# Performance work log

Measured on AMD Instinct MI355X. Metric: run time of the kernel, lower is better.

The kernel has to match this reference:

```python
import jax, jax.numpy as jnp
import numpy as np

N_NODES = 50000
N_EDGES = 800000
IN_F = 128
HID_F = 128
OUT_F = 128

def safediv(a, b):
    b = jnp.where(b == 0, jnp.ones_like(b), b)
    return a / b

def setup_inputs() -> dict:
    key = jax.random.key(0)
    ks = jax.random.split(key, 8)
    h = jax.random.normal(ks[0], (N_NODES, IN_F), dtype=jnp.float32)
    ppr_weight = jax.random.uniform(ks[1], (N_EDGES,), dtype=jnp.float32)
    Qw = jax.random.normal(ks[2], (HID_F, IN_F), dtype=jnp.float32) * (1.0 / np.sqrt(IN_F))
    Qb = jnp.zeros((HID_F,), dtype=jnp.float32)
    Ww = jax.random.normal(ks[3], (OUT_F, IN_F + HID_F), dtype=jnp.float32) * (1.0 / np.sqrt(IN_F + HID_F))
    Wb = jnp.zeros((OUT_F,), dtype=jnp.float32)
    src = jax.random.randint(ks[4], (N_EDGES,), 0, N_NODES, dtype=jnp.int64 if jax.config.jax_enable_x64 else jnp.int32)
    dst = jax.random.randint(ks[5], (N_EDGES,), 0, N_NODES, dtype=jnp.int64 if jax.config.jax_enable_x64 else jnp.int32)
    return {"h": h, "ppr_weight": ppr_weight, "Qw": Qw, "Qb": Qb, "Ww": Ww, "Wb": Wb, "src": src, "dst": dst}

def reference(h, ppr_weight, Qw, Qb, Ww, Wb, src, dst):
    # neighbor transform: Q(h) -> [N, HID_F]
    hq = h @ Qw.T + Qb
    # message: h_w = hq[src] * ppr_weight  (edge-weighted gather) [E, HID_F]
    msg = hq[src] * ppr_weight[:, None]
    # reduce: scatter-sum messages and weights onto dst nodes
    h_agg = jax.ops.segment_sum(msg, dst, num_segments=N_NODES)
    w = jax.ops.segment_sum(ppr_weight, dst, num_segments=N_NODES)
    # apply: PPR-weighted mean, concat, linear, leaky_relu, L2 normalize
    h_agg = safediv(h_agg, w[:, None])
    h_concat = jnp.concatenate([h, h_agg], axis=1)
    h_new = jax.nn.leaky_relu(h_concat @ Ww.T + Wb, negative_slope=0.01)
    norm = jnp.linalg.norm(h_new, axis=1, keepdims=True)
    return safediv(h_new, norm)
```

## Files before the change

kernel.cpp:

```cpp
#include <hip/hip_runtime.h>
#include <stdint.h>

#define N_NODES 50000
#define N_EDGES 800000
#define IN_F 128
#define HID_F 128
#define OUT_F 128
#define CAT_F 256

#define NB 256
#define CHUNK 3136
#define NBUCK 3125
#define BCAP 384

typedef __bf16 bf16x8 __attribute__((ext_vector_type(8)));
typedef float f32x4 __attribute__((ext_vector_type(4)));

__device__ __forceinline__ uint32_t f2b(float f) {
  uint32_t u = __float_as_uint(f);
  return (u + 0x7fffu + ((u >> 16) & 1u)) >> 16;
}

__global__ void __launch_bounds__(256) prep_hist_kernel(
    const int* __restrict__ dst, int* __restrict__ G, const float* __restrict__ h,
    const float* __restrict__ Qw, const float* __restrict__ Ww, uint16_t* __restrict__ hB,
    uint16_t* __restrict__ QwB, uint16_t* __restrict__ WwB) {
  if (blockIdx.x < NB) {
    __shared__ int hist[NBUCK];
    for (int k = threadIdx.x; k < NBUCK; k += 256) hist[k] = 0;
    __syncthreads();
    int b = blockIdx.x;
    int base = b * CHUNK;
    int end = (base + CHUNK < N_EDGES) ? (base + CHUNK) : N_EDGES;
    for (int i4 = base / 4 + threadIdx.x; i4 * 4 < end; i4 += 256) {
      int4 d4 = ((const int4*)dst)[i4];
      atomicAdd(&hist[d4.x >> 4], 1);
      atomicAdd(&hist[d4.y >> 4], 1);
      atomicAdd(&hist[d4.z >> 4], 1);
      atomicAdd(&hist[d4.w >> 4], 1);
    }
    __syncthreads();
    for (int k = threadIdx.x; k < NBUCK; k += 256) G[(size_t)b * NBUCK + k] = hist[k];
  } else {
    const int TOT4 = (N_NODES * IN_F + HID_F * IN_F + OUT_F * CAT_F) / 4;
    int i4 = (blockIdx.x - NB) * 256 + threadIdx.x;
    if (i4 >= TOT4) return;
    int base = i4 * 4;
    const float* srcp;
    uint16_t* dstp;
    int off;
    if (base < N_NODES * IN_F) {
      srcp = h; dstp = hB; off = base;
    } else if (base < N_NODES * IN_F + HID_F * IN_F) {
      srcp = Qw; dstp = QwB; off = base - N_NODES * IN_F;
    } else {
      srcp = Ww; dstp = WwB; off = base - N_NODES * IN_F - HID_F * IN_F;
    }
    float4 v = *(const float4*)(srcp + off);
    ushort4 o;
    o.x = (uint16_t)f2b(v.x); o.y = (uint16_t)f2b(v.y);
    o.z = (uint16_t)f2b(v.z); o.w = (uint16_t)f2b(v.w);
    *(ushort4*)(dstp + off) = o;
  }
}

__global__ void __launch_bounds__(256) colscan_kernel(int* __restrict__ G,
                                                      int* __restrict__ cnt) {
  int w = (blockIdx.x * 256 + (int)threadIdx.x) >> 6;
  if (w >= NBUCK) return;
  int lane = threadIdx.x & 63;
  int v0 = G[(size_t)(4 * lane + 0) * NBUCK + w];
  int v1 = G[(size_t)(4 * lane + 1) * NBUCK + w];
  int v2 = G[(size_t)(4 * lane + 2) * NBUCK + w];
  int v3 = G[(size_t)(4 * lane + 3) * NBUCK + w];
  int s = v0 + v1 + v2 + v3;
  int inc = s;
#pragma unroll
  for (int d = 1; d < 64; d <<= 1) {
    int x = __shfl_up(inc, d, 64);
    if (lane >= d) inc += x;
  }
  int exc = inc - s;
  G[(size_t)(4 * lane + 0) * NBUCK + w] = exc;
  G[(size_t)(4 * lane + 1) * NBUCK + w] = exc + v0;
  G[(size_t)(4 * lane + 2) * NBUCK + w] = exc + v0 + v1;
  G[(size_t)(4 * lane + 3) * NBUCK + w] = exc + v0 + v1 + v2;
  if (lane == 63) cnt[w] = inc;
}

__global__ void __launch_bounds__(256) scatter_kernel(
    const int* __restrict__ dst, const int* __restrict__ src, const float* __restrict__ ppr,
    const int* __restrict__ G, int2* __restrict__ rec) {
  __shared__ int cursor[NBUCK];
  int b = blockIdx.x;
  for (int k = threadIdx.x; k < NBUCK; k += 256)
    cursor[k] = k * BCAP + G[(size_t)b * NBUCK + k];
  __syncthreads();
  int base = b * CHUNK;
  int end = (base + CHUNK < N_EDGES) ? (base + CHUNK) : N_EDGES;
  for (int i4 = base / 4 + threadIdx.x; i4 * 4 < end; i4 += 256) {
    int4 d4 = ((const int4*)dst)[i4];
    int4 s4 = ((const int4*)src)[i4];
    float4 w4 = ((const float4*)ppr)[i4];
    int k, p;
    k = d4.x >> 4; p = atomicAdd(&cursor[k], 1);
    if (p < (k + 1) * BCAP) rec[p] = make_int2(s4.x | ((d4.x & 15) << 20), __float_as_int(w4.x));
    k = d4.y >> 4; p = atomicAdd(&cursor[k], 1);
    if (p < (k + 1) * BCAP) rec[p] = make_int2(s4.y | ((d4.y & 15) << 20), __float_as_int(w4.y));
    k = d4.z >> 4; p = atomicAdd(&cursor[k], 1);
    if (p < (k + 1) * BCAP) rec[p] = make_int2(s4.z | ((d4.z & 15) << 20), __float_as_int(w4.z));
    k = d4.w >> 4; p = atomicAdd(&cursor[k], 1);
    if (p < (k + 1) * BCAP) rec[p] = make_int2(s4.w | ((d4.w & 15) << 20), __float_as_int(w4.w));
  }
}

__global__ void __launch_bounds__(256, 4) agg_gemm2_kernel(
    const int2* __restrict__ rec, const int* __restrict__ cnt,
    const uint16_t* __restrict__ hB, const uint16_t* __restrict__ QwB,
    const float* __restrict__ Qb, const uint16_t* __restrict__ WwB,
    const float* __restrict__ Wb, float* __restrict__ out) {
  __shared__ int2 srec[BCAP];
  __shared__ uint4 hagg[16][17];
  __shared__ uint4 hq2[16][17];
  __shared__ int hist[16];
  __shared__ int noff[17];
  __shared__ int cur[16];
  __shared__ float wsum[16];
  __shared__ float ssp[4][16];
  int g = blockIdx.x;
  int t = threadIdx.x;
  if (t < 16) hist[t] = 0;
  __syncthreads();

  int len = cnt[g];
  len = (len < BCAP) ? len : BCAP;
  const int2* rbase = rec + (size_t)g * BCAP;

  int2 rc[2];
#pragma unroll
  for (int k = 0; k < 2; ++k) {
    int i = t + k * 256;
    if (i < len) {
      rc[k] = rbase[i];
      atomicAdd(&hist[rc[k].x >> 20], 1);
    }
  }
  __syncthreads();

  if (t < 16) {
    int v = hist[t];
    int inc = v;
#pragma unroll
    for (int d = 1; d < 16; d <<= 1) {
      int x = __shfl_up(inc, d, 64);
      if (t >= d) inc += x;
    }
    noff[t] = inc - v;
    cur[t] = inc - v;
    if (t == 15) noff[16] = inc;
  }
  __syncthreads();

#pragma unroll
  for (int k = 0; k < 2; ++k) {
    int i = t + k * 256;
    if (i < len) {
      int p = atomicAdd(&cur[rc[k].x >> 20], 1);
      srec[p] = rc[k];
    }
  }
  __syncthreads();

  {
    int gs = t >> 4, c = t & 15;
    const uint4* hb4 = (const uint4*)hB;
    int nl = gs;
    int nbeg = noff[nl], nend = noff[nl + 1];
    int last = nend - 1;
    float a[8];
#pragma unroll
    for (int j = 0; j < 8; ++j) a[j] = 0.f;
    float ws = 0.f;

    int2 rrA[4], rrB[4];
    uint4 uA[4], uB[4];

#define LOADB(E0, RR, UU)                                         \
  {                                                               \
    _Pragma("unroll") for (int j = 0; j < 4; ++j) {               \
      int i = (E0) + j;                                           \
      RR[j] = srec[(i < last) ? i : last];                        \
    }                                                             \
    _Pragma("unroll") for (int j = 0; j < 4; ++j)                 \
        UU[j] = hb4[(size_t)(RR[j].x & 0xFFFFF) * 16 + c];        \
  }

#define CONSB(E0, RR, UU)                                           \
  {                                                                 \
    _Pragma("unroll") for (int j = 0; j < 4; ++j) {                 \
      float w = ((E0) + j < nend) ? __int_as_float(RR[j].y) : 0.f;  \
      ws += w;                                                      \
      uint32_t x;                                                   \
      x = UU[j].x;                                                  \
      a[0] += w * __uint_as_float(x << 16);                         \
      a[1] += w * __uint_as_float(x & 0xffff0000u);                 \
      x = UU[j].y;                                                  \
      a[2] += w * __uint_as_float(x << 16);                         \
      a[3] += w * __uint_as_float(x & 0xffff0000u);                 \
      x = UU[j].z;                                                  \
      a[4] += w * __uint_as_float(x << 16);                         \
      a[5] += w * __uint_as_float(x & 0xffff0000u);                 \
      x = UU[j].w;                                                  \
      a[6] += w * __uint_as_float(x << 16);                         \
      a[7] += w * __uint_as_float(x & 0xffff0000u);                 \
    }                                                               \
  }

    int e = nbeg;
    if (e < nend) {
      LOADB(e, rrA, uA);
      while (true) {
        int eB = e + 4;
        if (eB < nend) {
          LOADB(eB, rrB, uB);
          CONSB(e, rrA, uA);
          int eA = eB + 4;
          if (eA < nend) {
            LOADB(eA, rrA, uA);
            CONSB(eB, rrB, uB);
            e = eA;
          } else {
            CONSB(eB, rrB, uB);
            break;
          }
        } else {
          CONSB(e, rrA, uA);
          break;
        }
      }
    }
#undef LOADB
#undef CONSB

    float dnm = (ws == 0.f) ? 1.f : ws;
    float inv = 1.f / dnm;
    uint4 o;
    o.x = f2b(a[0] * inv) | (f2b(a[1] * inv) << 16);
    o.y = f2b(a[2] * inv) | (f2b(a[3] * inv) << 16);
    o.z = f2b(a[4] * inv) | (f2b(a[5] * inv) << 16);
    o.w = f2b(a[6] * inv) | (f2b(a[7] * inv) << 16);
    hagg[nl][c] = o;
    if (c == 0) wsum[nl] = ws;
  }
  __syncthreads();

  int lane = t & 63, wv = t >> 6;
  int r = lane & 15, qd = lane >> 4;

#pragma unroll
  for (int tq = 0; tq < 2; ++tq) {
    int tt = wv * 2 + tq;
    f32x4 acc = (f32x4){0.f, 0.f, 0.f, 0.f};
#pragma unroll
    for (int kt = 0; kt < 4; ++kt) {
      bf16x8 av = *(const bf16x8*)&hagg[r][kt * 4 + qd];
      bf16x8 b = *(const bf16x8*)(QwB + (tt * 16 + r) * IN_F + kt * 32 + qd * 8);
      acc = __builtin_amdgcn_mfma_f32_16x16x32_bf16(av, b, acc, 0, 0, 0);
    }
    float qb = Qb[tt * 16 + r];
#pragma unroll
    for (int rr2 = 0; rr2 < 4; ++rr2) {
      int row = qd * 4 + rr2;
      float flag = (wsum[row] != 0.f) ? 1.f : 0.f;
      ((uint16_t*)&hq2[row][0])[tt * 16 + r] = (uint16_t)f2b(acc[rr2] + qb * flag);
    }
  }
  __syncthreads();

  int row0 = g * 16;
  f32x4 acc2[2];
  acc2[0] = (f32x4){0.f, 0.f, 0.f, 0.f};
  acc2[1] = (f32x4){0.f, 0.f, 0.f, 0.f};
  const uint16_t* aRow = hB + (size_t)(row0 + r) * IN_F + qd * 8;
#pragma unroll
  for (int kt = 0; kt < 8; ++kt) {
    bf16x8 av;
    if (kt < 4) {
      av = *(const bf16x8*)(aRow + kt * 32);
    } else {
      av = *(const bf16x8*)&hq2[r][(kt - 4) * 4 + qd];
    }
#pragma unroll
    for (int tq = 0; tq < 2; ++tq) {
      int tt = wv * 2 + tq;
      bf16x8 b = *(const bf16x8*)(WwB + (tt * 16 + r) * CAT_F + kt * 32 + qd * 8);
      acc2[tq] = __builtin_amdgcn_mfma_f32_16x16x32_bf16(av, b, acc2[tq], 0, 0, 0);
    }
  }
  float lv[2][4];
  float ss[4] = {0.f, 0.f, 0.f, 0.f};
#pragma unroll
  for (int tq = 0; tq < 2; ++tq) {
    int tt = wv * 2 + tq;
    float wb = Wb[tt * 16 + r];
#pragma unroll
    for (int rr2 = 0; rr2 < 4; ++rr2) {
      float v = acc2[tq][rr2] + wb;
      v = (v >= 0.f) ? v : 0.01f * v;
      lv[tq][rr2] = v;
      ss[rr2] += v * v;
    }
  }
#pragma unroll
  for (int rr2 = 0; rr2 < 4; ++rr2) {
    float s = ss[rr2];
    s += __shfl_xor(s, 1);
    s += __shfl_xor(s, 2);
    s += __shfl_xor(s, 4);
    s += __shfl_xor(s, 8);
    ss[rr2] = s;
  }
  if (r == 0) {
#pragma unroll
    for (int rr2 = 0; rr2 < 4; ++rr2) ssp[wv][qd * 4 + rr2] = ss[rr2];
  }
  __syncthreads();
#pragma unroll
  for (int rr2 = 0; rr2 < 4; ++rr2) {
    int row = qd * 4 + rr2;
    float tot = ssp[0][row] + ssp[1][row] + ssp[2][row] + ssp[3][row];
    float nr = sqrtf(tot);
    float inv = (nr == 0.f) ? 1.f : (1.f / nr);
    float* orow = out + (size_t)(row0 + row) * OUT_F;
#pragma unroll
    for (int tq = 0; tq < 2; ++tq) {
      int tt = wv * 2 + tq;
      orow[tt * 16 + r] = lv[tq][rr2] * inv;
    }
  }
}

extern "C" void kernel_launch(void* const* d_in, const int* in_sizes, int n_in,
                              void* d_out, int out_size, void* d_ws, size_t ws_size,
                              hipStream_t stream) {
  const float* h = (const float*)d_in[0];
  const float* ppr = (const float*)d_in[1];
  const float* Qw = (const float*)d_in[2];
  const float* Qb = (const float*)d_in[3];
  const float* Ww = (const float*)d_in[4];
  const float* Wb = (const float*)d_in[5];
  const int* src = (const int*)d_in[6];
  const int* dst = (const int*)d_in[7];
  float* out = (float*)d_out;

  char* ws = (char*)d_ws;
  size_t o = 0;
  auto alloc = [&](size_t bytes) {
    void* p = ws + o;
    o = (o + bytes + 255) & ~(size_t)255;
    return p;
  };
  uint16_t* hB = (uint16_t*)alloc((size_t)N_NODES * IN_F * 2);
  uint16_t* QwB = (uint16_t*)alloc((size_t)HID_F * IN_F * 2);
  uint16_t* WwB = (uint16_t*)alloc((size_t)OUT_F * CAT_F * 2);
  int* G = (int*)alloc((size_t)NB * NBUCK * 4);
  int* cnt = (int*)alloc((size_t)NBUCK * 4);
  int2* rec = (int2*)alloc((size_t)NBUCK * BCAP * 8);

  const int CONV_BLOCKS = ((N_NODES * IN_F + HID_F * IN_F + OUT_F * CAT_F) / 4 + 255) / 256;
  prep_hist_kernel<<<NB + CONV_BLOCKS, 256, 0, stream>>>(dst, G, h, Qw, Ww, hB, QwB, WwB);
  colscan_kernel<<<(NBUCK + 3) / 4, 256, 0, stream>>>(G, cnt);
  scatter_kernel<<<NB, 256, 0, stream>>>(dst, src, ppr, G, rec);
  agg_gemm2_kernel<<<NBUCK, 256, 0, stream>>>(rec, cnt, hB, QwB, Qb, WwB, Wb, out);
}
```

Baseline: 186.6 us.

## Split aggregation from GEMMs and rewrite column scan as serial per-thread loop

Splits the fused aggregate-and-GEMM kernel into two kernels. The aggregation kernel writes bf16 neighbour means and weight sums to global memory. A separate GEMM kernel computes 16 rows per wave across all 128 output columns, so the row norm needs no cross-wave shared-memory reduction. The column scan now uses one thread per bucket that walks all 256 partitions serially into a separate output buffer, replacing the wave-wide shuffle scan. The goal is better occupancy and simpler GEMM scheduling, at the cost of an extra global round trip for the aggregated features, an extra launch, and a longer serial scan.

```diff
diff --git a/kernel.cpp b/kernel.cpp
--- a/kernel.cpp
+++ b/kernel.cpp
@@ -64,37 +64,28 @@
   }
 }
 
-__global__ void __launch_bounds__(256) colscan_kernel(int* __restrict__ G,
+__global__ void __launch_bounds__(256) colscan_kernel(const int* __restrict__ G,
+                                                      int* __restrict__ Gs,
                                                       int* __restrict__ cnt) {
-  int w = (blockIdx.x * 256 + (int)threadIdx.x) >> 6;
+  int w = blockIdx.x * 256 + threadIdx.x;
   if (w >= NBUCK) return;
-  int lane = threadIdx.x & 63;
-  int v0 = G[(size_t)(4 * lane + 0) * NBUCK + w];
-  int v1 = G[(size_t)(4 * lane + 1) * NBUCK + w];
-  int v2 = G[(size_t)(4 * lane + 2) * NBUCK + w];
-  int v3 = G[(size_t)(4 * lane + 3) * NBUCK + w];
-  int s = v0 + v1 + v2 + v3;
-  int inc = s;
-#pragma unroll
-  for (int d = 1; d < 64; d <<= 1) {
-    int x = __shfl_up(inc, d, 64);
-    if (lane >= d) inc += x;
-  }
-  int exc = inc - s;
-  G[(size_t)(4 * lane + 0) * NBUCK + w] = exc;
-  G[(size_t)(4 * lane + 1) * NBUCK + w] = exc + v0;
-  G[(size_t)(4 * lane + 2) * NBUCK + w] = exc + v0 + v1;
-  G[(size_t)(4 * lane + 3) * NBUCK + w] = exc + v0 + v1 + v2;
-  if (lane == 63) cnt[w] = inc;
+  int s = 0;
+#pragma unroll 8
+  for (int p = 0; p < NB; ++p) {
+    int v = G[(size_t)p * NBUCK + w];
+    Gs[(size_t)p * NBUCK + w] = s;
+    s += v;
+  }
+  cnt[w] = s;
 }
 
 __global__ void __launch_bounds__(256) scatter_kernel(
     const int* __restrict__ dst, const int* __restrict__ src, const float* __restrict__ ppr,
-    const int* __restrict__ G, int2* __restrict__ rec) {
+    const int* __restrict__ Gs, int2* __restrict__ rec) {
   __shared__ int cursor[NBUCK];
   int b = blockIdx.x;
   for (int k = threadIdx.x; k < NBUCK; k += 256)
-    cursor[k] = k * BCAP + G[(size_t)b * NBUCK + k];
+    cursor[k] = k * BCAP + Gs[(size_t)b * NBUCK + k];
   __syncthreads();
   int base = b * CHUNK;
   int end = (base + CHUNK < N_EDGES) ? (base + CHUNK) : N_EDGES;
@@ -114,19 +105,14 @@
   }
 }
 
-__global__ void __launch_bounds__(256, 4) agg_gemm2_kernel(
+__global__ void __launch_bounds__(256) agg_kernel(
     const int2* __restrict__ rec, const int* __restrict__ cnt,
-    const uint16_t* __restrict__ hB, const uint16_t* __restrict__ QwB,
-    const float* __restrict__ Qb, const uint16_t* __restrict__ WwB,
-    const float* __restrict__ Wb, float* __restrict__ out) {
+    const uint16_t* __restrict__ hB, uint16_t* __restrict__ haggB,
+    float* __restrict__ wsumG) {
   __shared__ int2 srec[BCAP];
-  __shared__ uint4 hagg[16][17];
-  __shared__ uint4 hq2[16][17];
   __shared__ int hist[16];
   __shared__ int noff[17];
   __shared__ int cur[16];
-  __shared__ float wsum[16];
-  __shared__ float ssp[4][16];
   int g = blockIdx.x;
   int t = threadIdx.x;
   if (t < 16) hist[t] = 0;
@@ -249,94 +235,101 @@
     o.y = f2b(a[2] * inv) | (f2b(a[3] * inv) << 16);
     o.z = f2b(a[4] * inv) | (f2b(a[5] * inv) << 16);
     o.w = f2b(a[6] * inv) | (f2b(a[7] * inv) << 16);
-    hagg[nl][c] = o;
-    if (c == 0) wsum[nl] = ws;
-  }
-  __syncthreads();
-
-  int lane = t & 63, wv = t >> 6;
-  int r = lane & 15, qd = lane >> 4;
-
-#pragma unroll
-  for (int tq = 0; tq < 2; ++tq) {
-    int tt = wv * 2 + tq;
-    f32x4 acc = (f32x4){0.f, 0.f, 0.f, 0.f};
+    int node = g * 16 + nl;
+    ((uint4*)haggB)[(size_t)node * 16 + c] = o;
+    if (c == 0) wsumG[node] = ws;
+  }
+}
+
+__global__ void __launch_bounds__(256) qgemm2_kernel(
+    const uint16_t* __restrict__ haggB, const float* __restrict__ wsumG,
+    const uint16_t* __restrict__ hB, const uint16_t* __restrict__ QwB,
+    const float* __restrict__ Qb, const uint16_t* __restrict__ WwB,
+    const float* __restrict__ Wb, float* __restrict__ out) {
+  __shared__ uint4 hq2[4][16][17];
+  int t = threadIdx.x;
+  int wv = t >> 6, lane = t & 63;
+  int w = blockIdx.x * 4 + wv;
+  bool act = (w < NBUCK);
+  int row0 = act ? w * 16 : 0;
+  int rl = lane & 15, qd = lane >> 4;
+
+  if (act) {
+    f32x4 accq[8];
+#pragma unroll
+    for (int tt = 0; tt < 8; ++tt) accq[tt] = (f32x4){0.f, 0.f, 0.f, 0.f};
+    const uint16_t* aRow = haggB + (size_t)(row0 + rl) * HID_F + qd * 8;
 #pragma unroll
     for (int kt = 0; kt < 4; ++kt) {
-      bf16x8 av = *(const bf16x8*)&hagg[r][kt * 4 + qd];
-      bf16x8 b = *(const bf16x8*)(QwB + (tt * 16 + r) * IN_F + kt * 32 + qd * 8);
-      acc = __builtin_amdgcn_mfma_f32_16x16x32_bf16(av, b, acc, 0, 0, 0);
-    }
-    float qb = Qb[tt * 16 + r];
-#pragma unroll
-    for (int rr2 = 0; rr2 < 4; ++rr2) {
-      int row = qd * 4 + rr2;
-      float flag = (wsum[row] != 0.f) ? 1.f : 0.f;
-      ((uint16_t*)&hq2[row][0])[tt * 16 + r] = (uint16_t)f2b(acc[rr2] + qb * flag);
-    }
-  }
-  __syncthreads();
-
-  int row0 = g * 16;
-  f32x4 acc2[2];
-  acc2[0] = (f32x4){0.f, 0.f, 0.f, 0.f};
-  acc2[1] = (f32x4){0.f, 0.f, 0.f, 0.f};
-  const uint16_t* aRow = hB + (size_t)(row0 + r) * IN_F + qd * 8;
+      bf16x8 a = *(const bf16x8*)(aRow + kt * 32);
+#pragma unroll
+      for (int tt = 0; tt < 8; ++tt) {
+        bf16x8 b = *(const bf16x8*)(QwB + (tt * 16 + rl) * IN_F + kt * 32 + qd * 8);
+        accq[tt] = __builtin_amdgcn_mfma_f32_16x16x32_bf16(a, b, accq[tt], 0, 0, 0);
+      }
+    }
+    float fl[4];
+#pragma unroll
+    for (int j = 0; j < 4; ++j)
+      fl[j] = (wsumG[row0 + qd * 4 + j] != 0.f) ? 1.f : 0.f;
+#pragma unroll
+    for (int tt = 0; tt < 8; ++tt) {
+      float qb = Qb[tt * 16 + rl];
+#pragma unroll
+      for (int j = 0; j < 4; ++j) {
+        int row = qd * 4 + j;
+        ((uint16_t*)&hq2[wv][row][0])[tt * 16 + rl] =
+            (uint16_t)f2b(accq[tt][j] + qb * fl[j]);
+      }
+    }
+  }
+  __syncthreads();
+  if (!act) return;
+
+  f32x4 acc2[8];
+#pragma unroll
+  for (int tt = 0; tt < 8; ++tt) acc2[tt] = (f32x4){0.f, 0.f, 0.f, 0.f};
+  const uint16_t* aRow2 = hB + (size_t)(row0 + rl) * IN_F + qd * 8;
 #pragma unroll
   for (int kt = 0; kt < 8; ++kt) {
     bf16x8 av;
     if (kt < 4) {
-      av = *(const bf16x8*)(aRow + kt * 32);
+      av = *(const bf16x8*)(aRow2 + kt * 32);
     } else {
-      av = *(const bf16x8*)&hq2[r][(kt - 4) * 4 + qd];
-    }
-#pragma unroll
-    for (int tq = 0; tq < 2; ++tq) {
-      int tt = wv * 2 + tq;
-      bf16x8 b = *(const bf16x8*)(WwB + (tt * 16 + r) * CAT_F + kt * 32 + qd * 8);
-      acc2[tq] = __builtin_amdgcn_mfma_f32_16x16x32_bf16(av, b, acc2[tq], 0, 0, 0);
-    }
-  }
-  float lv[2][4];
+      av = *(const bf16x8*)&hq2[wv][rl][(kt - 4) * 4 + qd];
+    }
+#pragma unroll
+    for (int tt = 0; tt < 8; ++tt) {
+      bf16x8 b = *(const bf16x8*)(WwB + (tt * 16 + rl) * CAT_F + kt * 32 + qd * 8);
+      acc2[tt] = __builtin_amdgcn_mfma_f32_16x16x32_bf16(av, b, acc2[tt], 0, 0, 0);
+    }
+  }
+  float lv[8][4];
   float ss[4] = {0.f, 0.f, 0.f, 0.f};
 #pragma unroll
-  for (int tq = 0; tq < 2; ++tq) {
-    int tt = wv * 2 + tq;
-    float wb = Wb[tt * 16 + r];
-#pragma unroll
-    for (int rr2 = 0; rr2 < 4; ++rr2) {
-      float v = acc2[tq][rr2] + wb;
+  for (int tt = 0; tt < 8; ++tt) {
+    float wb = Wb[tt * 16 + rl];
+#pragma unroll
+    for (int j = 0; j < 4; ++j) {
+      float v = acc2[tt][j] + wb;
       v = (v >= 0.f) ? v : 0.01f * v;
-      lv[tq][rr2] = v;
-      ss[rr2] += v * v;
-    }
-  }
-#pragma unroll
-  for (int rr2 = 0; rr2 < 4; ++rr2) {
-    float s = ss[rr2];
+      lv[tt][j] = v;
+      ss[j] += v * v;
+    }
+  }
+#pragma unroll
+  for (int j = 0; j < 4; ++j) {
+    float s = ss[j];
     s += __shfl_xor(s, 1);
     s += __shfl_xor(s, 2);
     s += __shfl_xor(s, 4);
     s += __shfl_xor(s, 8);
-    ss[rr2] = s;
-  }
-  if (r == 0) {
-#pragma unroll
-    for (int rr2 = 0; rr2 < 4; ++rr2) ssp[wv][qd * 4 + rr2] = ss[rr2];
-  }
-  __syncthreads();
-#pragma unroll
-  for (int rr2 = 0; rr2 < 4; ++rr2) {
-    int row = qd * 4 + rr2;
-    float tot = ssp[0][row] + ssp[1][row] + ssp[2][row] + ssp[3][row];
-    float nr = sqrtf(tot);
+    float nr = sqrtf(s);
     float inv = (nr == 0.f) ? 1.f : (1.f / nr);
-    float* orow = out + (size_t)(row0 + row) * OUT_F;
-#pragma unroll
-    for (int tq = 0; tq < 2; ++tq) {
-      int tt = wv * 2 + tq;
-      orow[tt * 16 + r] = lv[tq][rr2] * inv;
-    }
+    int mrow = row0 + qd * 4 + j;
+    float* orow = out + (size_t)mrow * OUT_F;
+#pragma unroll
+    for (int tt = 0; tt < 8; ++tt) orow[tt * 16 + rl] = lv[tt][j] * inv;
   }
 }
 
@@ -361,15 +354,20 @@
     return p;
   };
   uint16_t* hB = (uint16_t*)alloc((size_t)N_NODES * IN_F * 2);
+  uint16_t* haggB = (uint16_t*)alloc((size_t)N_NODES * HID_F * 2);
   uint16_t* QwB = (uint16_t*)alloc((size_t)HID_F * IN_F * 2);
   uint16_t* WwB = (uint16_t*)alloc((size_t)OUT_F * CAT_F * 2);
+  float* wsumG = (float*)alloc((size_t)N_NODES * 4);
   int* G = (int*)alloc((size_t)NB * NBUCK * 4);
+  int* Gs = (int*)alloc((size_t)NB * NBUCK * 4);
   int* cnt = (int*)alloc((size_t)NBUCK * 4);
   int2* rec = (int2*)alloc((size_t)NBUCK * BCAP * 8);
 
   const int CONV_BLOCKS = ((N_NODES * IN_F + HID_F * IN_F + OUT_F * CAT_F) / 4 + 255) / 256;
   prep_hist_kernel<<<NB + CONV_BLOCKS, 256, 0, stream>>>(dst, G, h, Qw, Ww, hB, QwB, WwB);
-  colscan_kernel<<<(NBUCK + 3) / 4, 256, 0, stream>>>(G, cnt);
-  scatter_kernel<<<NB, 256, 0, stream>>>(dst, src, ppr, G, rec);
-  agg_gemm2_kernel<<<NBUCK, 256, 0, stream>>>(rec, cnt, hB, QwB, Qb, WwB, Wb, out);
-}
+  colscan_kernel<<<(NBUCK + 255) / 256, 256, 0, stream>>>(G, Gs, cnt);
+  scatter_kernel<<<NB, 256, 0, stream>>>(dst, src, ppr, Gs, rec);
+  agg_kernel<<<NBUCK, 256, 0, stream>>>(rec, cnt, hB, haggB, wsumG);
+  qgemm2_kernel<<<(NBUCK + 3) / 4, 256, 0, stream>>>(haggB, wsumG, hB, QwB, Qb, WwB, Wb,
+                                                     out);
+}
```

After: 209.6 us. +12.3%, slower.
